# Kernel tuning notes

Hardware: AMD Instinct MI355X
Metric: run time of the kernel (lower is better)

The kernel has to match this reference:

```python
import jax, jax.numpy as jnp
import numpy as np

N = 100000      # nodes
E = 1000000     # edges
G = 1024        # graphs
NODE_IN, CLIMBER_IN, HID, OUT, HEADS = 6, 4, 64, 4, 2
SLOPE = 0.2     # PyG GATConv default negative_slope


def gat_conv(x, edge_index, W, att_src, att_dst, bias):
    """PyG GATConv, heads=HEADS, concat=False (mean over heads), add_self_loops=True."""
    heads, ch = att_src.shape
    xp = (x @ W).reshape(-1, heads, ch)                       # [N,H,C]
    a_src = jnp.einsum('nhc,hc->nh', xp, att_src)             # [N,H]
    a_dst = jnp.einsum('nhc,hc->nh', xp, att_dst)
    loops = jnp.arange(x.shape[0])
    src = jnp.concatenate([edge_index[0], loops])             # [E+N]
    dst = jnp.concatenate([edge_index[1], loops])
    e = jax.nn.leaky_relu(a_src[src] + a_dst[dst], SLOPE)     # [E+N,H]
    emax = jax.ops.segment_max(e, dst, num_segments=x.shape[0])
    emax = jnp.where(jnp.isfinite(emax), emax, 0.0)
    ex = jnp.exp(e - emax[dst])
    den = jax.ops.segment_sum(ex, dst, num_segments=x.shape[0])
    alpha = ex / (den[dst] + 1e-16)                           # segment softmax over incoming edges
    msg = xp[src] * alpha[:, :, None]                         # [E+N,H,C]
    agg = jax.ops.segment_sum(msg, dst, num_segments=x.shape[0])  # [N,H,C]
    return agg.mean(axis=1) + bias                            # concat=False -> head mean


def setup_inputs() -> dict:
    key = jax.random.key(0)
    ks = jax.random.split(key, 20)
    s = lambda *d: 1.0 / np.sqrt(d[0])
    inp = {
        'x': jax.random.normal(ks[0], (N, NODE_IN), jnp.float32),
        'edge_index': jax.random.randint(ks[1], (2, E), 0, N),
        'batch': jnp.sort(jax.random.randint(ks[2], (N,), 0, G)),
        'climber': jax.random.normal(ks[3], (G, CLIMBER_IN), jnp.float32),
        # conv1 params
        'W1': jax.random.normal(ks[4], (NODE_IN, HEADS * HID), jnp.float32) * s(NODE_IN),
        'as1': jax.random.normal(ks[5], (HEADS, HID), jnp.float32) * s(HID),
        'ad1': jax.random.normal(ks[6], (HEADS, HID), jnp.float32) * s(HID),
        'b1': jnp.zeros((HID,), jnp.float32),
        # conv2 params
        'W2': jax.random.normal(ks[7], (HID, HEADS * HID), jnp.float32) * s(HID),
        'as2': jax.random.normal(ks[8], (HEADS, HID), jnp.float32) * s(HID),
        'ad2': jax.random.normal(ks[9], (HEADS, HID), jnp.float32) * s(HID),
        'b2': jnp.zeros((HID,), jnp.float32),
        # climber embed
        'Wc': jax.random.normal(ks[10], (CLIMBER_IN, HID), jnp.float32) * s(CLIMBER_IN),
        'bc': jnp.zeros((HID,), jnp.float32),
        # classifier
        'Wm1': jax.random.normal(ks[11], (2 * HID, HID), jnp.float32) * s(2 * HID),
        'bm1': jnp.zeros((HID,), jnp.float32),
        'Wm2': jax.random.normal(ks[12], (HID, OUT), jnp.float32) * s(HID),
        'bm2': jnp.zeros((OUT,), jnp.float32),
    }
    return inp


def reference(x, edge_index, batch, climber, W1, as1, ad1, b1, W2, as2, ad2, b2,
              Wc, bc, Wm1, bm1, Wm2, bm2):
    h = jax.nn.relu(gat_conv(x, edge_index, W1, as1, ad1, b1))
    h = jax.nn.relu(gat_conv(h, edge_index, W2, as2, ad2, b2))
    c = jax.nn.relu(climber @ Wc + bc)            # dropout is identity in eval mode
    z = jnp.concatenate([h, c[batch]], axis=1)    # [N, 2*HID]
    z = jax.nn.relu(z @ Wm1 + bm1)                # dropout identity (eval)
    return z @ Wm2 + bm2                          # [N, OUT]
```

## Files before the change

kernel.cpp:

```cpp
#include <hip/hip_runtime.h>
#include <hip/hip_fp16.h>

#define SLOPE 0.2f

__device__ __forceinline__ float lrelu(float v) { return v >= 0.f ? v : SLOPE * v; }

__device__ __forceinline__ unsigned pack2(float a, float b) {
    __half2 h = __floats2half2_rn(a, b);
    return *reinterpret_cast<unsigned*>(&h);
}
__device__ __forceinline__ float2 h2f(unsigned u) {
    __half2 h = *reinterpret_cast<__half2*>(&u);
    return __half22float2(h);
}

__device__ __forceinline__ void pk8(unsigned& A0, unsigned& A1, unsigned& A2, unsigned& A3,
                                    unsigned ap, uint4 u) {
    __half2 a = *reinterpret_cast<__half2*>(&ap);
    __half2* up = reinterpret_cast<__half2*>(&u);
    *reinterpret_cast<__half2*>(&A0) = __hfma2(up[0], a, *reinterpret_cast<__half2*>(&A0));
    *reinterpret_cast<__half2*>(&A1) = __hfma2(up[1], a, *reinterpret_cast<__half2*>(&A1));
    *reinterpret_cast<__half2*>(&A2) = __hfma2(up[2], a, *reinterpret_cast<__half2*>(&A2));
    *reinterpret_cast<__half2*>(&A3) = __hfma2(up[3], a, *reinterpret_cast<__half2*>(&A3));
}

__global__ __launch_bounds__(256)
void k_xp_gemm64h(const __half* __restrict__ x, const float* __restrict__ W,
                  const float* __restrict__ as_, const float* __restrict__ ad_,
                  __half* __restrict__ xph, float* __restrict__ asrc,
                  float* __restrict__ adst, int N) {
    constexpr int K = 64;
    constexpr int ZS = K + 1;
    __shared__ float zs[64 * ZS];
    __shared__ float ws[K * 128];
    const int n0 = blockIdx.x * 64;
    const int t = threadIdx.x;

    for (int i = t; i < K * 32; i += 256) ((float4*)ws)[i] = ((const float4*)W)[i];
    for (int i = t; i < 64 * 8; i += 256) {
        int n = i >> 3, k8 = i & 7;
        int gn = n0 + n;
        uint4 v = make_uint4(0u, 0u, 0u, 0u);
        if (gn < N) v = ((const uint4*)x)[(size_t)gn * 8 + k8];
        float2 f0 = h2f(v.x), f1 = h2f(v.y), f2 = h2f(v.z), f3 = h2f(v.w);
        float* zr = zs + n * ZS + k8 * 8;
        zr[0] = f0.x; zr[1] = f0.y; zr[2] = f1.x; zr[3] = f1.y;
        zr[4] = f2.x; zr[5] = f2.y; zr[6] = f3.x; zr[7] = f3.y;
    }
    __syncthreads();

    const int tx = t & 15, ty = t >> 4;
    const int c0a = tx * 4;
    const int c0b = 64 + tx * 4;

    float4 asA = *(const float4*)(as_ + c0a);
    float4 asB = *(const float4*)(as_ + c0b);
    float4 adA = *(const float4*)(ad_ + c0a);
    float4 adB = *(const float4*)(ad_ + c0b);

    float acc[4][8];
    #pragma unroll
    for (int i = 0; i < 4; ++i)
        #pragma unroll
        for (int j = 0; j < 8; ++j) acc[i][j] = 0.f;

    for (int k = 0; k < K; ++k) {
        float4 w0 = *(const float4*)(ws + k * 128 + c0a);
        float4 w1 = *(const float4*)(ws + k * 128 + c0b);
        #pragma unroll
        for (int i = 0; i < 4; ++i) {
            float zv = zs[(ty * 4 + i) * ZS + k];
            acc[i][0] += zv * w0.x; acc[i][1] += zv * w0.y;
            acc[i][2] += zv * w0.z; acc[i][3] += zv * w0.w;
            acc[i][4] += zv * w1.x; acc[i][5] += zv * w1.y;
            acc[i][6] += zv * w1.z; acc[i][7] += zv * w1.w;
        }
    }

    #pragma unroll
    for (int i = 0; i < 4; ++i) {
        int nl = ty * 4 + i, gn = n0 + nl;
        if (gn < N) {
            uint2 ua, ub;
            ua.x = pack2(acc[i][0], acc[i][1]);
            ua.y = pack2(acc[i][2], acc[i][3]);
            ub.x = pack2(acc[i][4], acc[i][5]);
            ub.y = pack2(acc[i][6], acc[i][7]);
            *(uint2*)(xph + (size_t)gn * 128 + c0a) = ua;
            *(uint2*)(xph + (size_t)gn * 128 + c0b) = ub;
        }
        float ps0 = acc[i][0]*asA.x + acc[i][1]*asA.y + acc[i][2]*asA.z + acc[i][3]*asA.w;
        float ps1 = acc[i][4]*asB.x + acc[i][5]*asB.y + acc[i][6]*asB.z + acc[i][7]*asB.w;
        float pd0 = acc[i][0]*adA.x + acc[i][1]*adA.y + acc[i][2]*adA.z + acc[i][3]*adA.w;
        float pd1 = acc[i][4]*adB.x + acc[i][5]*adB.y + acc[i][6]*adB.z + acc[i][7]*adB.w;
        #pragma unroll
        for (int off = 1; off <= 8; off <<= 1) {
            ps0 += __shfl_xor(ps0, off, 64);
            ps1 += __shfl_xor(ps1, off, 64);
            pd0 += __shfl_xor(pd0, off, 64);
            pd1 += __shfl_xor(pd1, off, 64);
        }
        if (tx == 0 && gn < N) {
            asrc[gn * 2]     = ps0;
            asrc[gn * 2 + 1] = ps1;
            adst[gn * 2]     = pd0;
            adst[gn * 2 + 1] = pd1;
        }
    }
}

__global__ void k_hist(const int* __restrict__ dst, int* __restrict__ deg,
                       int* __restrict__ rank, int E) {
    int e0 = (blockIdx.x * blockDim.x + threadIdx.x) * 4;
    if (e0 + 3 < E) {
        int4 d = *(const int4*)(dst + e0);
        int r0 = atomicAdd(&deg[d.x], 1);
        int r1 = atomicAdd(&deg[d.y], 1);
        int r2 = atomicAdd(&deg[d.z], 1);
        int r3 = atomicAdd(&deg[d.w], 1);
        *(int4*)(rank + e0) = make_int4(r0, r1, r2, r3);
    } else {
        for (int e = e0; e < E; ++e) rank[e] = atomicAdd(&deg[dst[e]], 1);
    }
}

__global__ void k_scan_partial(const int* __restrict__ deg, int* __restrict__ partial, int N) {
    int b = blockIdx.x, t = threadIdx.x;
    int base = b * 1024 + t * 4;
    int s = 0;
    for (int i = 0; i < 4; ++i) { int idx = base + i; if (idx < N) s += deg[idx]; }
    __shared__ int sh[256];
    sh[t] = s; __syncthreads();
    for (int off = 128; off > 0; off >>= 1) { if (t < off) sh[t] += sh[t + off]; __syncthreads(); }
    if (t == 0) partial[b] = sh[0];
}

__global__ void k_scan_final(const int* __restrict__ deg, const int* __restrict__ partial,
                             int* __restrict__ rowptr, int N, int E, int nb) {
    int b = blockIdx.x, t = threadIdx.x;
    __shared__ int shp[256];
    shp[t] = (t < nb) ? partial[t] : 0;
    __syncthreads();
    for (int off = 1; off < 256; off <<= 1) {
        int v = (t >= off) ? shp[t - off] : 0;
        __syncthreads();
        shp[t] += v;
        __syncthreads();
    }
    int pbase = (b > 0) ? shp[b - 1] : 0;
    __syncthreads();

    int base = b * 1024 + t * 4;
    int local[4]; int s = 0;
    for (int i = 0; i < 4; ++i) { int idx = base + i; local[i] = (idx < N) ? deg[idx] : 0; s += local[i]; }
    __shared__ int sh[256];
    int orig = s;
    sh[t] = s; __syncthreads();
    for (int off = 1; off < 256; off <<= 1) {
        int v = (t >= off) ? sh[t - off] : 0;
        __syncthreads();
        sh[t] += v;
        __syncthreads();
    }
    int run = pbase + sh[t] - orig;
    for (int i = 0; i < 4; ++i) {
        int idx = base + i;
        if (idx < N) rowptr[idx] = run;
        run += local[i];
    }
    if (b == 0 && t == 0) rowptr[N] = E;
}

__global__ __launch_bounds__(256)
void k_fused3(const int* __restrict__ srcI, const int* __restrict__ dstI,
              const int* __restrict__ rowptr, const int* __restrict__ rank,
              int* __restrict__ csr_src, int E,
              const float* __restrict__ x, const float* __restrict__ W1,
              const float* __restrict__ as1, const float* __restrict__ ad1,
              __half* __restrict__ xph, float* __restrict__ asrc,
              float* __restrict__ adst, int N,
              const float* __restrict__ climber, const float* __restrict__ Wc,
              const float* __restrict__ bc, const float* __restrict__ Wm1,
              const float* __restrict__ bm1, float* __restrict__ cpre, int G,
              int nEdgeBlk4, int nTile) {
    __shared__ float smem[4352];
    int bid = blockIdx.x;
    const int t = threadIdx.x;

    if (bid < nEdgeBlk4) {
        int e0 = (bid * 256 + t) * 4;
        if (e0 + 3 < E) {
            int4 s = *(const int4*)(srcI + e0);
            int4 d = *(const int4*)(dstI + e0);
            int4 r = *(const int4*)(rank + e0);
            int p0 = rowptr[d.x] + r.x;
            int p1 = rowptr[d.y] + r.y;
            int p2 = rowptr[d.z] + r.z;
            int p3 = rowptr[d.w] + r.w;
            csr_src[p0] = s.x;
            csr_src[p1] = s.y;
            csr_src[p2] = s.z;
            csr_src[p3] = s.w;
        } else {
            for (int e = e0; e < E; ++e)
                csr_src[rowptr[dstI[e]] + rank[e]] = srcI[e];
        }
        return;
    }
    bid -= nEdgeBlk4;
    if (bid < nTile) {
        constexpr int K = 6, ZS = 7;
        float* zs = smem;
        float* ws = smem + 448;
        const int n0 = bid * 64;

        for (int i = t; i < K * 32; i += 256) ((float4*)ws)[i] = ((const float4*)W1)[i];
        for (int i = t; i < 64 * K; i += 256) {
            int n = i / K, k = i - n * K;
            int gn = n0 + n;
            zs[n * ZS + k] = (gn < N) ? x[(size_t)gn * K + k] : 0.f;
        }
        __syncthreads();

        const int tx = t & 15, ty = t >> 4;
        const int c0a = tx * 4;
        const int c0b = 64 + tx * 4;

        float4 asA = *(const float4*)(as1 + c0a);
        float4 asB = *(const float4*)(as1 + c0b);
        float4 adA = *(const float4*)(ad1 + c0a);
        float4 adB = *(const float4*)(ad1 + c0b);

        float acc[4][8];
        #pragma unroll
        for (int i = 0; i < 4; ++i)
            #pragma unroll
            for (int j = 0; j < 8; ++j) acc[i][j] = 0.f;

        for (int k = 0; k < K; ++k) {
            float4 w0 = *(const float4*)(ws + k * 128 + c0a);
            float4 w1 = *(const float4*)(ws + k * 128 + c0b);
            #pragma unroll
            for (int i = 0; i < 4; ++i) {
                float zv = zs[(ty * 4 + i) * ZS + k];
                acc[i][0] += zv * w0.x; acc[i][1] += zv * w0.y;
                acc[i][2] += zv * w0.z; acc[i][3] += zv * w0.w;
                acc[i][4] += zv * w1.x; acc[i][5] += zv * w1.y;
                acc[i][6] += zv * w1.z; acc[i][7] += zv * w1.w;
            }
        }

        #pragma unroll
        for (int i = 0; i < 4; ++i) {
            int nl = ty * 4 + i, gn = n0 + nl;
            if (gn < N) {
                uint2 ua, ub;
                ua.x = pack2(acc[i][0], acc[i][1]);
                ua.y = pack2(acc[i][2], acc[i][3]);
                ub.x = pack2(acc[i][4], acc[i][5]);
                ub.y = pack2(acc[i][6], acc[i][7]);
                *(uint2*)(xph + (size_t)gn * 128 + c0a) = ua;
                *(uint2*)(xph + (size_t)gn * 128 + c0b) = ub;
            }
            float ps0 = acc[i][0]*asA.x + acc[i][1]*asA.y + acc[i][2]*asA.z + acc[i][3]*asA.w;
            float ps1 = acc[i][4]*asB.x + acc[i][5]*asB.y + acc[i][6]*asB.z + acc[i][7]*asB.w;
            float pd0 = acc[i][0]*adA.x + acc[i][1]*adA.y + acc[i][2]*adA.z + acc[i][3]*adA.w;
            float pd1 = acc[i][4]*adB.x + acc[i][5]*adB.y + acc[i][6]*adB.z + acc[i][7]*adB.w;
            #pragma unroll
            for (int off = 1; off <= 8; off <<= 1) {
                ps0 += __shfl_xor(ps0, off, 64);
                ps1 += __shfl_xor(ps1, off, 64);
                pd0 += __shfl_xor(pd0, off, 64);
                pd1 += __shfl_xor(pd1, off, 64);
            }
            if (tx == 0 && gn < N) {
                asrc[gn * 2]     = ps0;
                asrc[gn * 2 + 1] = ps1;
                adst[gn * 2]     = pd0;
                adst[gn * 2 + 1] = pd1;
            }
        }
        return;
    }
    bid -= nTile;
    {
        float* ce   = smem;
        float* wm1b = smem + 256;
        for (int i = t; i < 1024; i += 256) ((float4*)wm1b)[i] = ((const float4*)Wm1)[1024 + i];
        int gl = t >> 6, c = t & 63;
        int g = bid * 4 + gl;
        float acc = bc[c];
        if (g < G)
            for (int k = 0; k < 4; ++k) acc += climber[g * 4 + k] * Wc[k * 64 + c];
        ce[gl * 64 + c] = fmaxf(acc, 0.f);
        __syncthreads();
        float o = bm1[c];
        for (int k = 0; k < 64; ++k) o += ce[gl * 64 + k] * wm1b[k * 64 + c];
        if (g < G) cpre[(size_t)g * 64 + c] = o;
    }
}

__global__ void k_ag(const int* __restrict__ rowptr, const int* __restrict__ csr_src,
                     const float* __restrict__ asrc, const float* __restrict__ adst,
                     const __half* __restrict__ xph, const float* __restrict__ b,
                     __half* __restrict__ hout, int N) {
    int tid = blockIdx.x * blockDim.x + threadIdx.x;
    int lane = threadIdx.x & 63;
    int wid = tid >> 6;
    int nw = (gridDim.x * blockDim.x) >> 6;
    const int l  = lane & 31;
    const int hh = lane >> 5;
    const int g4 = (lane >> 3) & 3;
    const int c8 = lane & 7;
    const int lofs = hh * 8 + c8;
    const uint4* xp4 = (const uint4*)xph;
    float4 bb0 = ((const float4*)b)[c8 * 2];
    float4 bb1 = ((const float4*)b)[c8 * 2 + 1];

    for (int n = wid; n < N; n += nw) {
        int rs = rowptr[n], re = rowptr[n + 1], cnt = re - rs;
        uint4 uself = xp4[(size_t)n * 16 + lofs];
        float a_dst = adst[n * 2 + hh];
        float eself = __expf(lrelu(asrc[n * 2 + hh] + a_dst));

        unsigned A0 = 0u, A1 = 0u, A2 = 0u, A3 = 0u;
        float den;

        if (cnt <= 32) {
            float ev = 0.f; int s_reg = n;
            if (l < cnt) {
                s_reg = csr_src[rs + l];
                ev = __expf(lrelu(asrc[s_reg * 2 + hh] + a_dst));
            }
            unsigned evp = pack2(ev, ev);
            if (g4 == 0) pk8(A0, A1, A2, A3, pack2(eself, eself), uself);

            const int base = (hh << 5) - rs;
            int e0 = rs;
            for (; e0 + 4 < re; e0 += 8) {
                int ea = e0 + g4, eb = e0 + 4 + g4;
                unsigned aa = __shfl(evp,   base + ea, 64);
                int      sa = __shfl(s_reg, base + ea, 64);
                unsigned ab = __shfl(evp,   base + eb, 64);
                int      sb = __shfl(s_reg, base + eb, 64);
                if (eb >= re) { ab = 0u; sb = n; }
                uint4 u1 = xp4[(size_t)sa * 16 + lofs];
                uint4 u2 = xp4[(size_t)sb * 16 + lofs];
                pk8(A0, A1, A2, A3, aa, u1);
                pk8(A0, A1, A2, A3, ab, u2);
            }
            if (e0 < re) {
                int ea = e0 + g4;
                unsigned aa = __shfl(evp,   base + ea, 64);
                int      sa = __shfl(s_reg, base + ea, 64);
                if (ea >= re) { aa = 0u; sa = n; }
                uint4 u1 = xp4[(size_t)sa * 16 + lofs];
                pk8(A0, A1, A2, A3, aa, u1);
            }
            den = ev + (l == 0 ? eself : 0.f);
            #pragma unroll
            for (int off = 16; off > 0; off >>= 1) den += __shfl_xor(den, off, 64);
        } else {
            den = (l == 0) ? eself : 0.f;
            for (int e = rs + l; e < re; e += 32)
                den += __expf(lrelu(asrc[csr_src[e] * 2 + hh] + a_dst));
            #pragma unroll
            for (int off = 16; off > 0; off >>= 1) den += __shfl_xor(den, off, 64);
            if (g4 == 0) pk8(A0, A1, A2, A3, pack2(eself, eself), uself);
            for (int e0 = rs; e0 < re; e0 += 8) {
                int ea = e0 + g4, eb = e0 + 4 + g4;
                bool va = ea < re, vb = eb < re;
                int sa = va ? csr_src[ea] : n;
                int sb = vb ? csr_src[eb] : n;
                float fa = va ? __expf(lrelu(asrc[sa * 2 + hh] + a_dst)) : 0.f;
                float fb = vb ? __expf(lrelu(asrc[sb * 2 + hh] + a_dst)) : 0.f;
                unsigned aa = pack2(fa, fa);
                unsigned ab = pack2(fb, fb);
                uint4 u1 = xp4[(size_t)sa * 16 + lofs];
                uint4 u2 = xp4[(size_t)sb * 16 + lofs];
                pk8(A0, A1, A2, A3, aa, u1);
                pk8(A0, A1, A2, A3, ab, u2);
            }
        }

        float inv = 1.f / (den + 1e-16f);

        float2 f0 = h2f(A0), f1 = h2f(A1), f2 = h2f(A2), f3 = h2f(A3);
        float4 accA = make_float4(f0.x, f0.y, f1.x, f1.y);
        float4 accB = make_float4(f2.x, f2.y, f3.x, f3.y);

        #pragma unroll
        for (int off = 8; off <= 16; off <<= 1) {
            accA.x += __shfl_xor(accA.x, off, 64);
            accA.y += __shfl_xor(accA.y, off, 64);
            accA.z += __shfl_xor(accA.z, off, 64);
            accA.w += __shfl_xor(accA.w, off, 64);
            accB.x += __shfl_xor(accB.x, off, 64);
            accB.y += __shfl_xor(accB.y, off, 64);
            accB.z += __shfl_xor(accB.z, off, 64);
            accB.w += __shfl_xor(accB.w, off, 64);
        }
        accA.x *= inv; accA.y *= inv; accA.z *= inv; accA.w *= inv;
        accB.x *= inv; accB.y *= inv; accB.z *= inv; accB.w *= inv;
        accA.x += __shfl_xor(accA.x, 32, 64);
        accA.y += __shfl_xor(accA.y, 32, 64);
        accA.z += __shfl_xor(accA.z, 32, 64);
        accA.w += __shfl_xor(accA.w, 32, 64);
        accB.x += __shfl_xor(accB.x, 32, 64);
        accB.y += __shfl_xor(accB.y, 32, 64);
        accB.z += __shfl_xor(accB.z, 32, 64);
        accB.w += __shfl_xor(accB.w, 32, 64);

        if (lane < 8) {
            uint4 up;
            up.x = pack2(fmaxf(accA.x * 0.5f + bb0.x, 0.f),
                         fmaxf(accA.y * 0.5f + bb0.y, 0.f));
            up.y = pack2(fmaxf(accA.z * 0.5f + bb0.z, 0.f),
                         fmaxf(accA.w * 0.5f + bb0.w, 0.f));
            up.z = pack2(fmaxf(accB.x * 0.5f + bb1.x, 0.f),
                         fmaxf(accB.y * 0.5f + bb1.y, 0.f));
            up.w = pack2(fmaxf(accB.z * 0.5f + bb1.z, 0.f),
                         fmaxf(accB.w * 0.5f + bb1.w, 0.f));
            ((uint4*)hout)[(size_t)n * 8 + c8] = up;
        }
    }
}

__global__ __launch_bounds__(256)
void k_final(const __half* __restrict__ h2, const float* __restrict__ cpre,
             const int* __restrict__ batch, const float* __restrict__ Wm1,
             const float* __restrict__ Wm2, const float* __restrict__ bm2,
             float* __restrict__ out, int N) {
    __shared__ float zs[64 * 65];
    __shared__ float ws[64 * 64];
    __shared__ float4 w2l[64];
    const int n0 = blockIdx.x * 64;
    const int t = threadIdx.x;

    for (int i = t; i < 1024; i += 256) ((float4*)ws)[i] = ((const float4*)Wm1)[i];
    if (t < 64) w2l[t] = ((const float4*)Wm2)[t];
    for (int i = t; i < 64 * 8; i += 256) {
        int n = i >> 3, k8 = i & 7;
        int gn = n0 + n;
        uint4 v = make_uint4(0u, 0u, 0u, 0u);
        if (gn < N) v = ((const uint4*)h2)[(size_t)gn * 8 + k8];
        float2 f0 = h2f(v.x), f1 = h2f(v.y), f2 = h2f(v.z), f3 = h2f(v.w);
        float* zr = zs + n * 65 + k8 * 8;
        zr[0] = f0.x; zr[1] = f0.y; zr[2] = f1.x; zr[3] = f1.y;
        zr[4] = f2.x; zr[5] = f2.y; zr[6] = f3.x; zr[7] = f3.y;
    }
    __syncthreads();

    const int tx = t & 15, ty = t >> 4;
    const int c0 = tx * 4;
    float acc[4][4];
    #pragma unroll
    for (int i = 0; i < 4; ++i)
        #pragma unroll
        for (int j = 0; j < 4; ++j) acc[i][j] = 0.f;

    for (int k = 0; k < 64; ++k) {
        float4 wv = *(const float4*)(ws + k * 64 + c0);
        #pragma unroll
        for (int i = 0; i < 4; ++i) {
            float zv = zs[(ty * 4 + i) * 65 + k];
            acc[i][0] += zv * wv.x; acc[i][1] += zv * wv.y;
            acc[i][2] += zv * wv.z; acc[i][3] += zv * wv.w;
        }
    }
    __syncthreads();

    float4 wa = w2l[c0], wb = w2l[c0 + 1], wc = w2l[c0 + 2], wd = w2l[c0 + 3];
    #pragma unroll
    for (int i = 0; i < 4; ++i) {
        int nl = ty * 4 + i, gn = n0 + nl;
        float4 o = make_float4(0.f, 0.f, 0.f, 0.f);
        if (gn < N) {
            int b = batch[gn];
            float4 cp = *(const float4*)(cpre + (size_t)b * 64 + c0);
            float m0 = fmaxf(acc[i][0] + cp.x, 0.f);
            float m1 = fmaxf(acc[i][1] + cp.y, 0.f);
            float m2 = fmaxf(acc[i][2] + cp.z, 0.f);
            float m3 = fmaxf(acc[i][3] + cp.w, 0.f);
            o.x = m0 * wa.x + m1 * wb.x + m2 * wc.x + m3 * wd.x;
            o.y = m0 * wa.y + m1 * wb.y + m2 * wc.y + m3 * wd.y;
            o.z = m0 * wa.z + m1 * wb.z + m2 * wc.z + m3 * wd.z;
            o.w = m0 * wa.w + m1 * wb.w + m2 * wc.w + m3 * wd.w;
        }
        *(float4*)(zs + tx * 260 + nl * 4) = o;
    }
    __syncthreads();
    {
        int nl = t >> 2, j = t & 3, gn = n0 + nl;
        float s = 0.f;
        #pragma unroll
        for (int tx2 = 0; tx2 < 16; ++tx2) s += zs[tx2 * 260 + nl * 4 + j];
        if (gn < N) out[(size_t)gn * 4 + j] = s + bm2[j];
    }
}

extern "C" void kernel_launch(void* const* d_in, const int* in_sizes, int n_in,
                              void* d_out, int out_size, void* d_ws, size_t ws_size,
                              hipStream_t stream) {
    const float* x       = (const float*)d_in[0];
    const int*   ei      = (const int*)  d_in[1];
    const int*   batch   = (const int*)  d_in[2];
    const float* climber = (const float*)d_in[3];
    const float* W1  = (const float*)d_in[4];
    const float* as1 = (const float*)d_in[5];
    const float* ad1 = (const float*)d_in[6];
    const float* b1  = (const float*)d_in[7];
    const float* W2  = (const float*)d_in[8];
    const float* as2 = (const float*)d_in[9];
    const float* ad2 = (const float*)d_in[10];
    const float* b2  = (const float*)d_in[11];
    const float* Wc  = (const float*)d_in[12];
    const float* bc  = (const float*)d_in[13];
    const float* Wm1 = (const float*)d_in[14];
    const float* bm1 = (const float*)d_in[15];
    const float* Wm2 = (const float*)d_in[16];
    const float* bm2 = (const float*)d_in[17];

    const int N  = in_sizes[0] / 6;
    const int E  = in_sizes[1] / 2;
    const int G  = in_sizes[3] / 4;

    const int* srcI = ei;
    const int* dstI = ei + E;

    char* base = (char*)d_ws;
    size_t off = 0;
    auto carve = [&](size_t bytes) { void* p = base + off; off += (bytes + 255) & ~size_t(255); return p; };
    __half* xph   = (__half*)carve((size_t)N * 128 * 2);
    __half* hbuf  = (__half*)carve((size_t)N * 64 * 2);
    float* asrc   = (float*)carve((size_t)N * 2 * 4);
    float* adst   = (float*)carve((size_t)N * 2 * 4);
    float* cpre   = (float*)carve((size_t)G * 64 * 4);
    int*   deg    = (int*)  carve((size_t)N * 4);
    int*   rowptr = (int*)  carve((size_t)(N + 1) * 4);
    int*   rank   = (int*)  carve((size_t)E * 4);
    int*   partial= (int*)  carve(4096 * 4);
    int*   csr_src= (int*)  carve((size_t)E * 4);

    const int tpb = 256;
    const int nScanBlk = (N + 1023) / 1024;
    const int nEdgeBlk4 = (E + 1023) / 1024;
    const int nClimber = (G + 3) / 4;
    const int PG = 2048;
    const int nTile = (N + 63) / 64;

    hipMemsetAsync(deg, 0, (size_t)N * 4, stream);
    k_hist<<<nEdgeBlk4, tpb, 0, stream>>>(dstI, deg, rank, E);
    k_scan_partial<<<nScanBlk, tpb, 0, stream>>>(deg, partial, N);
    k_scan_final<<<nScanBlk, tpb, 0, stream>>>(deg, partial, rowptr, N, E, nScanBlk);
    k_fused3<<<nEdgeBlk4 + nTile + nClimber, tpb, 0, stream>>>(
        srcI, dstI, rowptr, rank, csr_src, E,
        x, W1, as1, ad1, xph, asrc, adst, N,
        climber, Wc, bc, Wm1, bm1, cpre, G, nEdgeBlk4, nTile);

    k_ag<<<PG, tpb, 0, stream>>>(rowptr, csr_src, asrc, adst, xph, b1, hbuf, N);

    k_xp_gemm64h<<<nTile, tpb, 0, stream>>>(hbuf, W2, as2, ad2, xph, asrc, adst, N);
    k_ag<<<PG, tpb, 0, stream>>>(rowptr, csr_src, asrc, adst, xph, b2, hbuf, N);

    k_final<<<nTile, tpb, 0, stream>>>(hbuf, cpre, batch, Wm1, Wm2, bm2, (float*)d_out, N);
}
```

Before: 317.1 us.

## Build CSR via two-level bucket partition with shared-memory atomics

Replaces the global-atomic histogram, scan and scatter used to build the CSR with a bucketed counting sort. Edges are first bucketed by destination in 512-node buckets using shared-memory counts. Each bucket's rowptr and csr_src are then built inside one block with local atomics. This aims to remove the heavy contention of a million global atomics and the random global scatter, at the cost of an extra 8-byte-per-edge staging buffer and more passes over the edges. It also assumes at most 256 buckets, so N is limited to about 131k nodes.

```diff
diff --git a/kernel.cpp b/kernel.cpp
--- a/kernel.cpp
+++ b/kernel.cpp
@@ -2,6 +2,9 @@
 #include <hip/hip_fp16.h>
 
 #define SLOPE 0.2f
+#define BKW  512
+#define BKSH 9
+#define MAXB 256
 
 __device__ __forceinline__ float lrelu(float v) { return v >= 0.f ? v : SLOPE * v; }
 
@@ -109,109 +112,160 @@
     }
 }
 
-__global__ void k_hist(const int* __restrict__ dst, int* __restrict__ deg,
-                       int* __restrict__ rank, int E) {
-    int e0 = (blockIdx.x * blockDim.x + threadIdx.x) * 4;
-    if (e0 + 3 < E) {
-        int4 d = *(const int4*)(dst + e0);
-        int r0 = atomicAdd(&deg[d.x], 1);
-        int r1 = atomicAdd(&deg[d.y], 1);
-        int r2 = atomicAdd(&deg[d.z], 1);
-        int r3 = atomicAdd(&deg[d.w], 1);
-        *(int4*)(rank + e0) = make_int4(r0, r1, r2, r3);
-    } else {
-        for (int e = e0; e < E; ++e) rank[e] = atomicAdd(&deg[dst[e]], 1);
-    }
-}
-
-__global__ void k_scan_partial(const int* __restrict__ deg, int* __restrict__ partial, int N) {
-    int b = blockIdx.x, t = threadIdx.x;
-    int base = b * 1024 + t * 4;
-    int s = 0;
-    for (int i = 0; i < 4; ++i) { int idx = base + i; if (idx < N) s += deg[idx]; }
+__global__ __launch_bounds__(256)
+void k_bcount(const int* __restrict__ dst, int* __restrict__ bkt_cnt, int E, int nb) {
+    __shared__ int cnt[MAXB];
+    int t = threadIdx.x;
+    for (int i = t; i < MAXB; i += 256) cnt[i] = 0;
+    __syncthreads();
+    int be = blockIdx.x * 4096;
+    int n = min(4096, E - be);
+    const int4* d4 = (const int4*)(dst + be);
+    #pragma unroll
+    for (int i = 0; i < 4; ++i) {
+        int j = t + 256 * i, r = j * 4;
+        if (r < n) {
+            int4 d = d4[j];
+            if (r + 0 < n) atomicAdd(&cnt[d.x >> BKSH], 1);
+            if (r + 1 < n) atomicAdd(&cnt[d.y >> BKSH], 1);
+            if (r + 2 < n) atomicAdd(&cnt[d.z >> BKSH], 1);
+            if (r + 3 < n) atomicAdd(&cnt[d.w >> BKSH], 1);
+        }
+    }
+    __syncthreads();
+    for (int b = t; b < nb; b += 256) if (cnt[b]) atomicAdd(&bkt_cnt[b], cnt[b]);
+}
+
+__global__ __launch_bounds__(256)
+void k_bscan(const int* __restrict__ bkt_cnt, int* __restrict__ bkt_base,
+             int* __restrict__ bkt_cur, int nb, int E) {
     __shared__ int sh[256];
-    sh[t] = s; __syncthreads();
-    for (int off = 128; off > 0; off >>= 1) { if (t < off) sh[t] += sh[t + off]; __syncthreads(); }
-    if (t == 0) partial[b] = sh[0];
-}
-
-__global__ void k_scan_final(const int* __restrict__ deg, const int* __restrict__ partial,
-                             int* __restrict__ rowptr, int N, int E, int nb) {
-    int b = blockIdx.x, t = threadIdx.x;
-    __shared__ int shp[256];
-    shp[t] = (t < nb) ? partial[t] : 0;
-    __syncthreads();
+    int t = threadIdx.x;
+    int v = (t < nb) ? bkt_cnt[t] : 0;
+    int orig = v;
+    sh[t] = v; __syncthreads();
     for (int off = 1; off < 256; off <<= 1) {
-        int v = (t >= off) ? shp[t - off] : 0;
-        __syncthreads();
-        shp[t] += v;
-        __syncthreads();
-    }
-    int pbase = (b > 0) ? shp[b - 1] : 0;
-    __syncthreads();
-
-    int base = b * 1024 + t * 4;
-    int local[4]; int s = 0;
-    for (int i = 0; i < 4; ++i) { int idx = base + i; local[i] = (idx < N) ? deg[idx] : 0; s += local[i]; }
+        int u = (t >= off) ? sh[t - off] : 0;
+        __syncthreads(); sh[t] += u; __syncthreads();
+    }
+    int base = sh[t] - orig;
+    if (t < nb) { bkt_base[t] = base; bkt_cur[t] = base; }
+    if (t == 0) bkt_base[nb] = E;
+}
+
+__global__ __launch_bounds__(256)
+void k_part(const int* __restrict__ src, const int* __restrict__ dst,
+            int* __restrict__ bkt_cur, uint2* __restrict__ ebuf, int E) {
+    __shared__ int cnt[MAXB];
+    __shared__ int shift[MAXB];
+    __shared__ int cur[MAXB];
     __shared__ int sh[256];
-    int orig = s;
-    sh[t] = s; __syncthreads();
+    __shared__ uint2 data[4096];
+    __shared__ unsigned char bof[4096];
+    int t = threadIdx.x;
+    cnt[t] = 0;
+    __syncthreads();
+    int be = blockIdx.x * 4096;
+    int n = min(4096, E - be);
+    const int4* d4 = (const int4*)(dst + be);
+    const int4* s4 = (const int4*)(src + be);
+    #pragma unroll
+    for (int i = 0; i < 4; ++i) {
+        int j = t + 256 * i, r = j * 4;
+        if (r < n) {
+            int4 d = d4[j];
+            if (r + 0 < n) atomicAdd(&cnt[d.x >> BKSH], 1);
+            if (r + 1 < n) atomicAdd(&cnt[d.y >> BKSH], 1);
+            if (r + 2 < n) atomicAdd(&cnt[d.z >> BKSH], 1);
+            if (r + 3 < n) atomicAdd(&cnt[d.w >> BKSH], 1);
+        }
+    }
+    __syncthreads();
+    int v = cnt[t], orig = v;
+    sh[t] = v; __syncthreads();
     for (int off = 1; off < 256; off <<= 1) {
-        int v = (t >= off) ? sh[t - off] : 0;
-        __syncthreads();
-        sh[t] += v;
-        __syncthreads();
-    }
-    int run = pbase + sh[t] - orig;
+        int u = (t >= off) ? sh[t - off] : 0;
+        __syncthreads(); sh[t] += u; __syncthreads();
+    }
+    int lb = sh[t] - orig;
+    cur[t] = lb;
+    if (orig > 0) {
+        int g = atomicAdd(&bkt_cur[t], orig);
+        shift[t] = g - lb;
+    }
+    __syncthreads();
+    #pragma unroll
     for (int i = 0; i < 4; ++i) {
-        int idx = base + i;
-        if (idx < N) rowptr[idx] = run;
-        run += local[i];
-    }
-    if (b == 0 && t == 0) rowptr[N] = E;
+        int j = t + 256 * i, r = j * 4;
+        if (r < n) {
+            int4 d = d4[j]; int4 s = s4[j];
+            if (r + 0 < n) { int b = d.x >> BKSH; int p = atomicAdd(&cur[b], 1); data[p] = make_uint2((unsigned)s.x, (unsigned)d.x); bof[p] = (unsigned char)b; }
+            if (r + 1 < n) { int b = d.y >> BKSH; int p = atomicAdd(&cur[b], 1); data[p] = make_uint2((unsigned)s.y, (unsigned)d.y); bof[p] = (unsigned char)b; }
+            if (r + 2 < n) { int b = d.z >> BKSH; int p = atomicAdd(&cur[b], 1); data[p] = make_uint2((unsigned)s.z, (unsigned)d.z); bof[p] = (unsigned char)b; }
+            if (r + 3 < n) { int b = d.w >> BKSH; int p = atomicAdd(&cur[b], 1); data[p] = make_uint2((unsigned)s.w, (unsigned)d.w); bof[p] = (unsigned char)b; }
+        }
+    }
+    __syncthreads();
+    for (int j = t; j < n; j += 256) {
+        int b = bof[j];
+        ebuf[shift[b] + j] = data[j];
+    }
 }
 
 __global__ __launch_bounds__(256)
-void k_fused3(const int* __restrict__ srcI, const int* __restrict__ dstI,
-              const int* __restrict__ rowptr, const int* __restrict__ rank,
-              int* __restrict__ csr_src, int E,
-              const float* __restrict__ x, const float* __restrict__ W1,
-              const float* __restrict__ as1, const float* __restrict__ ad1,
-              __half* __restrict__ xph, float* __restrict__ asrc,
-              float* __restrict__ adst, int N,
-              const float* __restrict__ climber, const float* __restrict__ Wc,
-              const float* __restrict__ bc, const float* __restrict__ Wm1,
-              const float* __restrict__ bm1, float* __restrict__ cpre, int G,
-              int nEdgeBlk4, int nTile) {
-    __shared__ float smem[4352];
+void k_build(const uint2* __restrict__ ebuf, const int* __restrict__ bkt_base,
+             int* __restrict__ rowptr, int* __restrict__ csr_src, int N, int E, int nb,
+             const float* __restrict__ x, const float* __restrict__ W1,
+             const float* __restrict__ as1, const float* __restrict__ ad1,
+             __half* __restrict__ xph, float* __restrict__ asrc,
+             float* __restrict__ adst,
+             const float* __restrict__ climber, const float* __restrict__ Wc,
+             const float* __restrict__ bc, const float* __restrict__ Wm1,
+             const float* __restrict__ bm1, float* __restrict__ cpre, int G,
+             int nTile) {
+    __shared__ char smem[17408];
+    __shared__ int sh[256];
     int bid = blockIdx.x;
     const int t = threadIdx.x;
 
-    if (bid < nEdgeBlk4) {
-        int e0 = (bid * 256 + t) * 4;
-        if (e0 + 3 < E) {
-            int4 s = *(const int4*)(srcI + e0);
-            int4 d = *(const int4*)(dstI + e0);
-            int4 r = *(const int4*)(rank + e0);
-            int p0 = rowptr[d.x] + r.x;
-            int p1 = rowptr[d.y] + r.y;
-            int p2 = rowptr[d.z] + r.z;
-            int p3 = rowptr[d.w] + r.w;
-            csr_src[p0] = s.x;
-            csr_src[p1] = s.y;
-            csr_src[p2] = s.z;
-            csr_src[p3] = s.w;
-        } else {
-            for (int e = e0; e < E; ++e)
-                csr_src[rowptr[dstI[e]] + rank[e]] = srcI[e];
-        }
+    if (bid < nb) {
+        int* deg = (int*)smem;
+        int* pre = deg + 512;
+        int* cur = pre + 512;
+        int n0 = bid << BKSH;
+        int nn = min(BKW, N - n0);
+        int eb = bkt_base[bid], ee = bkt_base[bid + 1];
+        for (int i = t; i < BKW; i += 256) deg[i] = 0;
+        __syncthreads();
+        for (int j = eb + t; j < ee; j += 256)
+            atomicAdd(&deg[(int)ebuf[j].y - n0], 1);
+        __syncthreads();
+        int a = deg[2 * t], b2 = deg[2 * t + 1];
+        int s = a + b2, orig = s;
+        sh[t] = s; __syncthreads();
+        for (int off = 1; off < 256; off <<= 1) {
+            int u = (t >= off) ? sh[t - off] : 0;
+            __syncthreads(); sh[t] += u; __syncthreads();
+        }
+        int base = sh[t] - orig;
+        pre[2 * t] = base; pre[2 * t + 1] = base + a;
+        cur[2 * t] = base; cur[2 * t + 1] = base + a;
+        __syncthreads();
+        for (int i = t; i < nn; i += 256) rowptr[n0 + i] = eb + pre[i];
+        for (int j = eb + t; j < ee; j += 256) {
+            uint2 e = ebuf[j];
+            int lp = atomicAdd(&cur[(int)e.y - n0], 1);
+            csr_src[eb + lp] = (int)e.x;
+        }
+        if (bid == 0 && t == 0) rowptr[N] = E;
         return;
     }
-    bid -= nEdgeBlk4;
+    bid -= nb;
     if (bid < nTile) {
         constexpr int K = 6, ZS = 7;
-        float* zs = smem;
-        float* ws = smem + 448;
+        float* smf = (float*)smem;
+        float* zs = smf;
+        float* ws = smf + 448;
         const int n0 = bid * 64;
 
         for (int i = t; i < K * 32; i += 256) ((float4*)ws)[i] = ((const float4*)W1)[i];
@@ -284,8 +338,9 @@
     }
     bid -= nTile;
     {
-        float* ce   = smem;
-        float* wm1b = smem + 256;
+        float* smf = (float*)smem;
+        float* ce   = smf;
+        float* wm1b = smf + 256;
         for (int i = t; i < 1024; i += 256) ((float4*)wm1b)[i] = ((const float4*)Wm1)[1024 + i];
         int gl = t >> 6, c = t & 63;
         int g = bid * 4 + gl;
@@ -531,32 +586,33 @@
     char* base = (char*)d_ws;
     size_t off = 0;
     auto carve = [&](size_t bytes) { void* p = base + off; off += (bytes + 255) & ~size_t(255); return p; };
-    __half* xph   = (__half*)carve((size_t)N * 128 * 2);
-    __half* hbuf  = (__half*)carve((size_t)N * 64 * 2);
-    float* asrc   = (float*)carve((size_t)N * 2 * 4);
-    float* adst   = (float*)carve((size_t)N * 2 * 4);
-    float* cpre   = (float*)carve((size_t)G * 64 * 4);
-    int*   deg    = (int*)  carve((size_t)N * 4);
-    int*   rowptr = (int*)  carve((size_t)(N + 1) * 4);
-    int*   rank   = (int*)  carve((size_t)E * 4);
-    int*   partial= (int*)  carve(4096 * 4);
-    int*   csr_src= (int*)  carve((size_t)E * 4);
+    __half* xph    = (__half*)carve((size_t)N * 128 * 2);
+    __half* hbuf   = (__half*)carve((size_t)N * 64 * 2);
+    float* asrc    = (float*)carve((size_t)N * 2 * 4);
+    float* adst    = (float*)carve((size_t)N * 2 * 4);
+    float* cpre    = (float*)carve((size_t)G * 64 * 4);
+    int*   rowptr  = (int*)  carve((size_t)(N + 1) * 4);
+    int*   csr_src = (int*)  carve((size_t)E * 4);
+    uint2* ebuf    = (uint2*)carve((size_t)E * 8);
+    int*   bkt_cnt = (int*)  carve((size_t)MAXB * 4);
+    int*   bkt_base= (int*)  carve((size_t)(MAXB + 1) * 4);
+    int*   bkt_cur = (int*)  carve((size_t)MAXB * 4);
 
     const int tpb = 256;
-    const int nScanBlk = (N + 1023) / 1024;
-    const int nEdgeBlk4 = (E + 1023) / 1024;
+    const int nb = (N + BKW - 1) >> BKSH;
+    const int nChunk = (E + 4095) / 4096;
     const int nClimber = (G + 3) / 4;
     const int PG = 2048;
     const int nTile = (N + 63) / 64;
 
-    hipMemsetAsync(deg, 0, (size_t)N * 4, stream);
-    k_hist<<<nEdgeBlk4, tpb, 0, stream>>>(dstI, deg, rank, E);
-    k_scan_partial<<<nScanBlk, tpb, 0, stream>>>(deg, partial, N);
-    k_scan_final<<<nScanBlk, tpb, 0, stream>>>(deg, partial, rowptr, N, E, nScanBlk);
-    k_fused3<<<nEdgeBlk4 + nTile + nClimber, tpb, 0, stream>>>(
-        srcI, dstI, rowptr, rank, csr_src, E,
-        x, W1, as1, ad1, xph, asrc, adst, N,
-        climber, Wc, bc, Wm1, bm1, cpre, G, nEdgeBlk4, nTile);
+    hipMemsetAsync(bkt_cnt, 0, (size_t)nb * 4, stream);
+    k_bcount<<<nChunk, tpb, 0, stream>>>(dstI, bkt_cnt, E, nb);
+    k_bscan<<<1, tpb, 0, stream>>>(bkt_cnt, bkt_base, bkt_cur, nb, E);
+    k_part<<<nChunk, tpb, 0, stream>>>(srcI, dstI, bkt_cur, ebuf, E);
+    k_build<<<nb + nTile + nClimber, tpb, 0, stream>>>(
+        ebuf, bkt_base, rowptr, csr_src, N, E, nb,
+        x, W1, as1, ad1, xph, asrc, adst,
+        climber, Wc, bc, Wm1, bm1, cpre, G, nTile);
 
     k_ag<<<PG, tpb, 0, stream>>>(rowptr, csr_src, asrc, adst, xph, b1, hbuf, N);
 
```

After: 281.0 us. 11.4% less time.
